# Kernel optimization log

Measured on AMD Instinct MI355X. Metric: run time of the kernel, lower is better.

## Reference

```python
import jax, jax.numpy as jnp
import numpy as np

D_MODEL = 1024
N_HEAD = 16
D_HEAD = D_MODEL // N_HEAD


def setup_inputs() -> dict:
    key = jax.random.key(0)
    k_x, k_wqkv, k_bqkv, k_wp, k_bp = jax.random.split(key, 5)
    B, T = 2, 2048
    bound = 1.0 / np.sqrt(D_MODEL)
    return {
        "x": jax.random.normal(k_x, (B, T, D_MODEL), dtype=jnp.float32),
        "w_qkv": jax.random.uniform(k_wqkv, (D_MODEL, 3 * D_MODEL), jnp.float32, -bound, bound),
        "b_qkv": jax.random.uniform(k_bqkv, (3 * D_MODEL,), jnp.float32, -bound, bound),
        "w_proj": jax.random.uniform(k_wp, (D_MODEL, D_MODEL), jnp.float32, -bound, bound),
        "b_proj": jax.random.uniform(k_bp, (D_MODEL,), jnp.float32, -bound, bound),
    }


def reference(x, w_qkv, b_qkv, w_proj, b_proj):
    B, T, C = x.shape
    qkv = x @ w_qkv + b_qkv                       # [B,T,3C]
    qkv = qkv.reshape(B, T, 3, N_HEAD, D_HEAD)
    qkv = jnp.transpose(qkv, (2, 0, 3, 1, 4))      # [3,B,H,T,dh]
    q, k, v = qkv[0], qkv[1], qkv[2]
    scale = np.sqrt(D_HEAD).astype(np.float32)
    attn = jnp.einsum("bhqd,bhkd->bhqk", q, k) / scale  # [B,H,T,T]
    causal = jnp.tril(jnp.ones((T, T), dtype=bool))
    attn = jnp.where(causal, attn, -jnp.inf)
    attn = jax.nn.softmax(attn, axis=-1)
    out = jnp.einsum("bhqk,bhkd->bhqd", attn, v)   # [B,H,T,dh]
    out = jnp.transpose(out, (0, 2, 1, 3)).reshape(B, T, C)
    return out @ w_proj + b_proj
```

## Files before the change

kernel.cpp:

```cpp
#include <hip/hip_runtime.h>
#include <hip/hip_bf16.h>
#include <math.h>

constexpr int Bb   = 2;
constexpr int T    = 2048;
constexpr int C    = 1024;
constexpr int H    = 16;
constexpr int M    = Bb * T;
constexpr int NQKV = 3 * C;

typedef __attribute__((ext_vector_type(8))) short bf16x8;
typedef __attribute__((ext_vector_type(4))) float f32x4;

__device__ inline short f2bf(float f) {
    __hip_bfloat16 h = __float2bfloat16(f);
    return *reinterpret_cast<short*>(&h);
}

#if __has_builtin(__builtin_amdgcn_exp2f)
#define EXP2(x) __builtin_amdgcn_exp2f(x)
#else
#define EXP2(x) exp2f(x)
#endif

#define GLOBAL_AS __attribute__((address_space(1)))
#define LDS_AS    __attribute__((address_space(3)))

__device__ __forceinline__ void gload_lds16(const short* g, short* s) {
    __builtin_amdgcn_global_load_lds((const GLOBAL_AS void*)g, (LDS_AS void*)s, 16, 0, 0);
}

__global__ __launch_bounds__(256)
void prep_all(const float* __restrict__ x, short* __restrict__ xb,
              const float* __restrict__ w_qkv, short* __restrict__ wqkvt,
              const float* __restrict__ w_proj, short* __restrict__ wprojt)
{
    __shared__ float tile[32][33];
    const int blk = blockIdx.x;
    const int tid = threadIdx.x;

    if (blk < 4096) {
        const int i = blk * 1024 + tid * 4;
        const float4 v = *(const float4*)(x + i);
        short4 s;
        s.x = f2bf(v.x); s.y = f2bf(v.y); s.z = f2bf(v.z); s.w = f2bf(v.w);
        *(short4*)(xb + i) = s;
        return;
    }

    const bool isqkv = (blk < 7168);
    const int bidx = isqkv ? (blk - 4096) : (blk - 7168);
    const int nblk = isqkv ? 96 : 32;
    const int N    = isqkv ? NQKV : C;
    const float* W = isqkv ? w_qkv : w_proj;
    short* Wt      = isqkv ? wqkvt : wprojt;

    const int n0 = (bidx % nblk) * 32, k0 = (bidx / nblk) * 32;
    const int tx = tid & 31, ty = tid >> 5;
#pragma unroll
    for (int i = 0; i < 32; i += 8)
        tile[ty + i][tx] = W[(size_t)(k0 + ty + i) * N + n0 + tx];
    __syncthreads();
#pragma unroll
    for (int i = 0; i < 32; i += 8)
        Wt[(size_t)(n0 + ty + i) * C + k0 + tx] = f2bf(tile[tx][ty + i]);
}

__global__ __launch_bounds__(256)
void gemm_mfma(const short* __restrict__ A, const short* __restrict__ Bt,
               const float* __restrict__ bias, short* __restrict__ outp,
               int Ndim, int Kdim)
{
    __shared__ __align__(16) short As[2 * 128 * 32];
    __shared__ __align__(16) short Bs[2 * 128 * 32];

    const int tid = threadIdx.x;
    const int w   = tid >> 6;
    const int l   = tid & 63;
    const int lk  = l & 15;
    const int lq  = l >> 4;

    const int gx  = gridDim.x;
    const int nwg = gx * gridDim.y;
    const int cpx = nwg >> 3;
    const int bid = blockIdx.y * gx + blockIdx.x;
    const int swz = (bid & 7) * cpx + (bid >> 3);
    const int m0  = (swz / gx) * 128;
    const int n0  = (swz % gx) * 128;

    const int mw  = (w >> 1) * 64, nw = (w & 1) * 64;

    const int srow = w * 16 + (l >> 2);
    const int scol = (l & 3) * 8;

    const short* agp0 = A  + (size_t)(m0 + srow)      * Kdim + scol;
    const short* agp1 = A  + (size_t)(m0 + 64 + srow) * Kdim + scol;
    const short* bgp0 = Bt + (size_t)(n0 + srow)      * Kdim + scol;
    const short* bgp1 = Bt + (size_t)(n0 + 64 + srow) * Kdim + scol;

    short* ad0 = &As[w * 512];
    short* ad1 = &As[2048 + w * 512];
    short* bd0 = &Bs[w * 512];
    short* bd1 = &Bs[2048 + w * 512];

    f32x4 acc[4][4];
#pragma unroll
    for (int i = 0; i < 4; ++i)
#pragma unroll
        for (int j = 0; j < 4; ++j) acc[i][j] = (f32x4){0.f, 0.f, 0.f, 0.f};

    gload_lds16(agp0, ad0);
    gload_lds16(agp1, ad1);
    gload_lds16(bgp0, bd0);
    gload_lds16(bgp1, bd1);
    __syncthreads();

    int cur = 0;
    for (int k0 = 0; k0 < Kdim; k0 += 32) {
        const int coff = cur ? 4096 : 0;

        bf16x8 af[4], bfr[4];
#pragma unroll
        for (int mt = 0; mt < 4; ++mt)
            af[mt] = *(const bf16x8*)&As[coff + (mw + mt * 16 + lk) * 32 + lq * 8];
#pragma unroll
        for (int nt = 0; nt < 4; ++nt)
            bfr[nt] = *(const bf16x8*)&Bs[coff + (nw + nt * 16 + lk) * 32 + lq * 8];

        if (k0 + 32 < Kdim) {
            const int noff = cur ? 0 : 4096;
            gload_lds16(agp0 + k0 + 32, ad0 + noff);
            gload_lds16(agp1 + k0 + 32, ad1 + noff);
            gload_lds16(bgp0 + k0 + 32, bd0 + noff);
            gload_lds16(bgp1 + k0 + 32, bd1 + noff);
        }

#pragma unroll
        for (int mt = 0; mt < 4; ++mt)
#pragma unroll
            for (int nt = 0; nt < 4; ++nt)
                acc[mt][nt] = __builtin_amdgcn_mfma_f32_16x16x32_bf16(bfr[nt], af[mt], acc[mt][nt], 0, 0, 0);

        __syncthreads();
        cur ^= 1;
    }

    float4 bv[4];
#pragma unroll
    for (int nt = 0; nt < 4; ++nt)
        bv[nt] = *(const float4*)(bias + n0 + nw + nt * 16 + lq * 4);
#pragma unroll
    for (int mt = 0; mt < 4; ++mt) {
        short* rowp = outp + (size_t)(m0 + mw + mt * 16 + lk) * Ndim + n0 + nw + lq * 4;
#pragma unroll
        for (int nt = 0; nt < 4; ++nt) {
            short4 pk;
            pk.x = f2bf(acc[mt][nt][0] + bv[nt].x);
            pk.y = f2bf(acc[mt][nt][1] + bv[nt].y);
            pk.z = f2bf(acc[mt][nt][2] + bv[nt].z);
            pk.w = f2bf(acc[mt][nt][3] + bv[nt].w);
            *(short4*)(rowp + nt * 16) = pk;
        }
    }
}

__global__ __launch_bounds__(256)
void gemm_mfma_proj(const short* __restrict__ A, const short* __restrict__ Bt,
                    const float* __restrict__ bias, float* __restrict__ outp,
                    int Ndim, int Kdim)
{
    __shared__ __align__(16) short As[2 * 64 * 32];
    __shared__ __align__(16) short Bs[2 * 128 * 32];

    const int tid = threadIdx.x;
    const int w   = tid >> 6;
    const int l   = tid & 63;
    const int lk  = l & 15;
    const int lq  = l >> 4;

    const int gx  = gridDim.x;
    const int nwg = gx * gridDim.y;
    const int cpx = nwg >> 3;
    const int bid = blockIdx.y * gx + blockIdx.x;
    const int swz = (bid & 7) * cpx + (bid >> 3);
    const int m0  = (swz / gx) * 64;
    const int n0  = (swz % gx) * 128;

    const int mw  = (w & 1) * 32, nw = (w >> 1) * 64;

    const int srow = w * 16 + (l >> 2);
    const int scol = (l & 3) * 8;

    const short* agp  = A  + (size_t)(m0 + srow)      * Kdim + scol;
    const short* bgp0 = Bt + (size_t)(n0 + srow)      * Kdim + scol;
    const short* bgp1 = Bt + (size_t)(n0 + 64 + srow) * Kdim + scol;

    short* ad  = &As[w * 512];
    short* bd0 = &Bs[w * 512];
    short* bd1 = &Bs[2048 + w * 512];

    f32x4 acc[2][4];
#pragma unroll
    for (int i = 0; i < 2; ++i)
#pragma unroll
        for (int j = 0; j < 4; ++j) acc[i][j] = (f32x4){0.f, 0.f, 0.f, 0.f};

    gload_lds16(agp,  ad);
    gload_lds16(bgp0, bd0);
    gload_lds16(bgp1, bd1);
    __syncthreads();

    int cur = 0;
    for (int k0 = 0; k0 < Kdim; k0 += 32) {
        const int coffA = cur ? 2048 : 0;
        const int coffB = cur ? 4096 : 0;

        bf16x8 af[2], bfr[4];
#pragma unroll
        for (int mt = 0; mt < 2; ++mt)
            af[mt] = *(const bf16x8*)&As[coffA + (mw + mt * 16 + lk) * 32 + lq * 8];
#pragma unroll
        for (int nt = 0; nt < 4; ++nt)
            bfr[nt] = *(const bf16x8*)&Bs[coffB + (nw + nt * 16 + lk) * 32 + lq * 8];

        if (k0 + 32 < Kdim) {
            const int noffA = cur ? 0 : 2048;
            const int noffB = cur ? 0 : 4096;
            gload_lds16(agp  + k0 + 32, ad  + noffA);
            gload_lds16(bgp0 + k0 + 32, bd0 + noffB);
            gload_lds16(bgp1 + k0 + 32, bd1 + noffB);
        }

#pragma unroll
        for (int mt = 0; mt < 2; ++mt)
#pragma unroll
            for (int nt = 0; nt < 4; ++nt)
                acc[mt][nt] = __builtin_amdgcn_mfma_f32_16x16x32_bf16(bfr[nt], af[mt], acc[mt][nt], 0, 0, 0);

        __syncthreads();
        cur ^= 1;
    }

    float4 bv[4];
#pragma unroll
    for (int nt = 0; nt < 4; ++nt)
        bv[nt] = *(const float4*)(bias + n0 + nw + nt * 16 + lq * 4);
#pragma unroll
    for (int mt = 0; mt < 2; ++mt) {
        float* rowp = outp + (size_t)(m0 + mw + mt * 16 + lk) * Ndim + n0 + nw + lq * 4;
#pragma unroll
        for (int nt = 0; nt < 4; ++nt) {
            float4 v;
            v.x = acc[mt][nt][0] + bv[nt].x;
            v.y = acc[mt][nt][1] + bv[nt].y;
            v.z = acc[mt][nt][2] + bv[nt].z;
            v.w = acc[mt][nt][3] + bv[nt].w;
            *(float4*)(rowp + nt * 16) = v;
        }
    }
}

constexpr int LDV = 136;
constexpr float SC = 0.18033688f;

__global__ __launch_bounds__(512, 2)
void attn_mfma(const short* __restrict__ qkv, short* __restrict__ att)
{
    __shared__ __align__(16) short Ks[2][128 * 64];
    __shared__ __align__(16) short Vt[2][64 * LDV];

    const int idx = blockIdx.x;
    const int xcd = idx & 7;
    const int r   = idx >> 3;
    const int bh  = xcd * 4 + (r & 3);
    const int s   = r >> 2;
    const int b   = bh >> 4;
    const int h   = bh & 15;

    const int tid = threadIdx.x;
    const int w   = tid >> 6;
    const int l   = tid & 63;
    const int lk  = l & 15;
    const int lq  = l >> 4;

    const short* base = qkv + (size_t)b * T * 3072 + h * 64;

    const int kcolsw = 8 * ((l & 7) ^ (l >> 3));
    const int swz    = lk & 15 & 7;

    const int k2  = tid & 63;
    const int vd0 = (tid >> 6) * 8;
    const int kk   = (2 * k2) & 31;
    const int vcol = ((2 * k2) >> 5) * 32 + ((kk >> 2) & 3) * 8
                   + ((kk >> 4) & 1) * 4 + (kk & 3);

    uint4 va, vb;

    for (int pi = 0; pi < 2; ++pi) {
        const int qt    = pi ? (15 - s) : s;
        const int qbase = qt * 128;
        const int nkt   = qt + 1;

        const int q_abs = qbase + w * 16 + lk;
        const short* qp = base + (size_t)q_abs * 3072 + lq * 8;
        const bf16x8 qf0 = *(const bf16x8*)qp;
        const bf16x8 qf1 = *(const bf16x8*)(qp + 32);

        f32x4 acc_o[4];
#pragma unroll
        for (int dt = 0; dt < 4; ++dt) acc_o[dt] = (f32x4){0.f, 0.f, 0.f, 0.f};
        float m_run = -INFINITY;
        float l_run = 0.f;

        __syncthreads();
#pragma unroll
        for (int rr = 0; rr < 2; ++rr) {
            const int rowbase = rr * 64 + w * 8;
            gload_lds16(base + 1024 + (size_t)(rowbase + (l >> 3)) * 3072 + kcolsw,
                        &Ks[0][rowbase * 64]);
        }
        {
            const short* vp = base + 2048 + (size_t)(2 * k2) * 3072 + vd0;
            va = *(const uint4*)vp;
            vb = *(const uint4*)(vp + 3072);
            const unsigned int Aa[4] = {va.x, va.y, va.z, va.w};
            const unsigned int Bbv[4] = {vb.x, vb.y, vb.z, vb.w};
#pragma unroll
            for (int p = 0; p < 4; ++p) {
                const unsigned int ue = (Aa[p] & 0xffffu) | (Bbv[p] << 16);
                const unsigned int uo = (Aa[p] >> 16) | (Bbv[p] & 0xffff0000u);
                *(unsigned int*)&Vt[0][(vd0 + 2 * p)     * LDV + vcol] = ue;
                *(unsigned int*)&Vt[0][(vd0 + 2 * p + 1) * LDV + vcol] = uo;
            }
        }
        __syncthreads();

#pragma unroll 1
        for (int it = 0; it < nkt; ++it) {
            const int j0  = it * 128;
            const int buf = it & 1;
            const int nb  = buf ^ 1;

            if (it + 1 < nkt) {
                const int j1 = j0 + 128;
#pragma unroll
                for (int rr = 0; rr < 2; ++rr) {
                    const int rowbase = rr * 64 + w * 8;
                    gload_lds16(base + 1024 + (size_t)(j1 + rowbase + (l >> 3)) * 3072 + kcolsw,
                                &Ks[nb][rowbase * 64]);
                }
                const short* vp = base + 2048 + (size_t)(j1 + 2 * k2) * 3072 + vd0;
                va = *(const uint4*)vp;
                vb = *(const uint4*)(vp + 3072);
            }

            f32x4 s4[8];
            __builtin_amdgcn_s_setprio(1);
#pragma unroll
            for (int kt = 0; kt < 8; ++kt) {
                const int row = kt * 16 + lk;
                const bf16x8 kf0 = *(const bf16x8*)&Ks[buf][row * 64 + 8 * (lq ^ swz)];
                const bf16x8 kf1 = *(const bf16x8*)&Ks[buf][row * 64 + 8 * ((lq + 4) ^ swz)];
                f32x4 a = (f32x4){0.f, 0.f, 0.f, 0.f};
                a = __builtin_amdgcn_mfma_f32_16x16x32_bf16(kf0, qf0, a, 0, 0, 0);
                a = __builtin_amdgcn_mfma_f32_16x16x32_bf16(kf1, qf1, a, 0, 0, 0);
                s4[kt] = a;
            }
            __builtin_amdgcn_s_setprio(0);

            if (it == nkt - 1) {
#pragma unroll
                for (int kt = 0; kt < 8; ++kt)
#pragma unroll
                    for (int r2 = 0; r2 < 4; ++r2)
                        if (j0 + kt * 16 + lq * 4 + r2 > q_abs) s4[kt][r2] = -1e30f;
            }

            float tm[8];
#pragma unroll
            for (int kt = 0; kt < 8; ++kt)
                tm[kt] = fmaxf(fmaxf(s4[kt][0], s4[kt][1]), fmaxf(s4[kt][2], s4[kt][3]));
            float mx = fmaxf(fmaxf(fmaxf(tm[0], tm[1]), fmaxf(tm[2], tm[3])),
                             fmaxf(fmaxf(tm[4], tm[5]), fmaxf(tm[6], tm[7])));
            mx = fmaxf(mx, __shfl_xor(mx, 16));
            mx = fmaxf(mx, __shfl_xor(mx, 32));

            const bool grow = __any(mx > m_run);
            float corr = 1.f;
            if (grow) {
                const float mn = fmaxf(m_run, mx);
                corr = EXP2((m_run - mn) * SC);
                m_run = mn;
            }
            const float nmc = -m_run * SC;
#pragma unroll
            for (int kt = 0; kt < 8; ++kt)
#pragma unroll
                for (int r2 = 0; r2 < 4; ++r2)
                    s4[kt][r2] = EXP2(fmaf(s4[kt][r2], SC, nmc));

            float ts[8];
#pragma unroll
            for (int kt = 0; kt < 8; ++kt)
                ts[kt] = (s4[kt][0] + s4[kt][1]) + (s4[kt][2] + s4[kt][3]);
            float ps = ((ts[0] + ts[1]) + (ts[2] + ts[3]))
                     + ((ts[4] + ts[5]) + (ts[6] + ts[7]));
            ps += __shfl_xor(ps, 16);
            ps += __shfl_xor(ps, 32);
            l_run = grow ? (l_run * corr + ps) : (l_run + ps);

            unsigned int d0[8], d1[8];
#pragma unroll
            for (int kt = 0; kt < 8; ++kt) {
                d0[kt] = (unsigned int)(unsigned short)f2bf(s4[kt][0])
                       | ((unsigned int)(unsigned short)f2bf(s4[kt][1]) << 16);
                d1[kt] = (unsigned int)(unsigned short)f2bf(s4[kt][2])
                       | ((unsigned int)(unsigned short)f2bf(s4[kt][3]) << 16);
            }

            if (grow) {
#pragma unroll
                for (int dt = 0; dt < 4; ++dt)
#pragma unroll
                    for (int r2 = 0; r2 < 4; ++r2) acc_o[dt][r2] *= corr;
            }

            __builtin_amdgcn_s_setprio(1);
#pragma unroll
            for (int kc = 0; kc < 4; ++kc) {
                union { unsigned int u[4]; bf16x8 v; } up;
                up.u[0] = d0[kc * 2];
                up.u[1] = d1[kc * 2];
                up.u[2] = d0[kc * 2 + 1];
                up.u[3] = d1[kc * 2 + 1];
                const bf16x8 pf = up.v;
#pragma unroll
                for (int dt = 0; dt < 4; ++dt) {
                    const bf16x8 vf = *(const bf16x8*)&Vt[buf][(dt * 16 + lk) * LDV + kc * 32 + lq * 8];
                    acc_o[dt] = __builtin_amdgcn_mfma_f32_16x16x32_bf16(vf, pf, acc_o[dt], 0, 0, 0);
                }
            }
            __builtin_amdgcn_s_setprio(0);

            if (it + 1 < nkt) {
                const unsigned int Aa[4] = {va.x, va.y, va.z, va.w};
                const unsigned int Bbv[4] = {vb.x, vb.y, vb.z, vb.w};
#pragma unroll
                for (int p = 0; p < 4; ++p) {
                    const unsigned int ue = (Aa[p] & 0xffffu) | (Bbv[p] << 16);
                    const unsigned int uo = (Aa[p] >> 16) | (Bbv[p] & 0xffff0000u);
                    *(unsigned int*)&Vt[nb][(vd0 + 2 * p)     * LDV + vcol] = ue;
                    *(unsigned int*)&Vt[nb][(vd0 + 2 * p + 1) * LDV + vcol] = uo;
                }
            }

            __syncthreads();
        }

        const float inv = 1.f / l_run;
        short* op = att + ((size_t)(b * T + q_abs)) * 1024 + h * 64;
#pragma unroll
        for (int dt = 0; dt < 4; ++dt) {
            short4 pk;
            pk.x = f2bf(acc_o[dt][0] * inv);
            pk.y = f2bf(acc_o[dt][1] * inv);
            pk.z = f2bf(acc_o[dt][2] * inv);
            pk.w = f2bf(acc_o[dt][3] * inv);
            *(short4*)(op + dt * 16 + lq * 4) = pk;
        }
    }
}

extern "C" void kernel_launch(void* const* d_in, const int* in_sizes, int n_in,
                              void* d_out, int out_size, void* d_ws, size_t ws_size,
                              hipStream_t stream)
{
    const float* x      = (const float*)d_in[0];
    const float* w_qkv  = (const float*)d_in[1];
    const float* b_qkv  = (const float*)d_in[2];
    const float* w_proj = (const float*)d_in[3];
    const float* b_proj = (const float*)d_in[4];
    float* out = (float*)d_out;

    short* xb     = (short*)d_ws;
    short* wqkvt  = xb     + (size_t)M * C;
    short* wprojt = wqkvt  + (size_t)NQKV * C;
    short* qkvb   = wprojt + (size_t)C * C;
    short* attb   = qkvb   + (size_t)M * NQKV;

    prep_all<<<8192, 256, 0, stream>>>(x, xb, w_qkv, wqkvt, w_proj, wprojt);
    gemm_mfma<<<dim3(NQKV / 128, M / 128), 256, 0, stream>>>(xb, wqkvt, b_qkv, qkvb, NQKV, C);
    attn_mfma<<<256, 512, 0, stream>>>(qkvb, attb);
    gemm_mfma_proj<<<dim3(C / 128, M / 64), 256, 0, stream>>>(attb, wprojt, b_proj, out, C, C);
}
```

Baseline: 188.0 us.

## Rewrite attention with 32x32x16 MFMA, 4-wave blocks, one q-tile per block

Switches the attention kernel from 16x16x32 to 32x32x16 bf16 MFMA, so each wave owns 32 query rows. Blocks shrink to 256 threads, and the grid doubles to 512 so each block handles one q-tile instead of a balanced pair. The V transpose into LDS now uses an XOR swizzle with no padding, and row reductions need fewer cross-lane shuffles. The goal is to cut LDS traffic and shuffle overhead per FLOP. In exchange, the pairing that balanced causal work within a block is lost and register pressure per wave rises.

```diff
diff --git a/kernel.cpp b/kernel.cpp
--- a/kernel.cpp
+++ b/kernel.cpp
@@ -11,6 +11,7 @@
 
 typedef __attribute__((ext_vector_type(8))) short bf16x8;
 typedef __attribute__((ext_vector_type(4))) float f32x4;
+typedef __attribute__((ext_vector_type(16))) float f32x16;
 
 __device__ inline short f2bf(float f) {
     __hip_bfloat16 h = __float2bfloat16(f);
@@ -260,215 +261,229 @@
     }
 }
 
-constexpr int LDV = 136;
 constexpr float SC = 0.18033688f;
 
-__global__ __launch_bounds__(512, 2)
+__global__ __launch_bounds__(256, 2)
 void attn_mfma(const short* __restrict__ qkv, short* __restrict__ att)
 {
     __shared__ __align__(16) short Ks[2][128 * 64];
-    __shared__ __align__(16) short Vt[2][64 * LDV];
-
-    const int idx = blockIdx.x;
-    const int xcd = idx & 7;
-    const int r   = idx >> 3;
-    const int bh  = xcd * 4 + (r & 3);
-    const int s   = r >> 2;
-    const int b   = bh >> 4;
-    const int h   = bh & 15;
+    __shared__ __align__(16) short Vt[2][64 * 128];
+
+    const int idx  = blockIdx.x;
+    const int half = idx >> 8;
+    const int i    = idx & 255;
+    const int xcd  = i & 7;
+    const int bh   = xcd * 4 + ((i >> 3) & 3);
+    const int s    = i >> 5;
+    const int qt   = half ? (15 - s) : s;
+    const int b    = bh >> 4;
+    const int h    = bh & 15;
+    const int qbase = qt * 128;
+    const int nkt   = qt + 1;
 
     const int tid = threadIdx.x;
     const int w   = tid >> 6;
     const int l   = tid & 63;
-    const int lk  = l & 15;
-    const int lq  = l >> 4;
+    const int c31 = l & 31;
+    const int hi  = l >> 5;
 
     const short* base = qkv + (size_t)b * T * 3072 + h * 64;
 
-    const int kcolsw = 8 * ((l & 7) ^ (l >> 3));
-    const int swz    = lk & 15 & 7;
-
-    const int k2  = tid & 63;
-    const int vd0 = (tid >> 6) * 8;
-    const int kk   = (2 * k2) & 31;
-    const int vcol = ((2 * k2) >> 5) * 32 + ((kk >> 2) & 3) * 8
-                   + ((kk >> 4) & 1) * 4 + (kk & 3);
-
-    uint4 va, vb;
-
-    for (int pi = 0; pi < 2; ++pi) {
-        const int qt    = pi ? (15 - s) : s;
-        const int qbase = qt * 128;
-        const int nkt   = qt + 1;
-
-        const int q_abs = qbase + w * 16 + lk;
-        const short* qp = base + (size_t)q_abs * 3072 + lq * 8;
-        const bf16x8 qf0 = *(const bf16x8*)qp;
-        const bf16x8 qf1 = *(const bf16x8*)(qp + 32);
-
-        f32x4 acc_o[4];
-#pragma unroll
-        for (int dt = 0; dt < 4; ++dt) acc_o[dt] = (f32x4){0.f, 0.f, 0.f, 0.f};
-        float m_run = -INFINITY;
-        float l_run = 0.f;
-
-        __syncthreads();
-#pragma unroll
-        for (int rr = 0; rr < 2; ++rr) {
-            const int rowbase = rr * 64 + w * 8;
-            gload_lds16(base + 1024 + (size_t)(rowbase + (l >> 3)) * 3072 + kcolsw,
-                        &Ks[0][rowbase * 64]);
-        }
-        {
-            const short* vp = base + 2048 + (size_t)(2 * k2) * 3072 + vd0;
-            va = *(const uint4*)vp;
-            vb = *(const uint4*)(vp + 3072);
-            const unsigned int Aa[4] = {va.x, va.y, va.z, va.w};
-            const unsigned int Bbv[4] = {vb.x, vb.y, vb.z, vb.w};
-#pragma unroll
-            for (int p = 0; p < 4; ++p) {
-                const unsigned int ue = (Aa[p] & 0xffffu) | (Bbv[p] << 16);
-                const unsigned int uo = (Aa[p] >> 16) | (Bbv[p] & 0xffff0000u);
-                *(unsigned int*)&Vt[0][(vd0 + 2 * p)     * LDV + vcol] = ue;
-                *(unsigned int*)&Vt[0][(vd0 + 2 * p + 1) * LDV + vcol] = uo;
+    const int q_abs = qbase + w * 32 + c31;
+    const short* qp = base + (size_t)q_abs * 3072 + hi * 8;
+    bf16x8 qf[4];
+#pragma unroll
+    for (int ds = 0; ds < 4; ++ds)
+        qf[ds] = *(const bf16x8*)(qp + ds * 16);
+
+    f32x16 acc_o[2];
+#pragma unroll
+    for (int dt = 0; dt < 2; ++dt)
+#pragma unroll
+        for (int r = 0; r < 16; ++r) acc_o[dt][r] = 0.f;
+    float m_run = -INFINITY;
+    float lacc  = 0.f;
+
+    const int kswz = 8 * ((l & 7) ^ ((l >> 3) & 7));
+
+    const int k0v = 2 * l;
+    const int kk5 = k0v & 31;
+    const int pos = (k0v >> 5) * 32 + ((kk5 >> 4) & 1) * 16 + ((kk5 >> 2) & 1) * 8
+                  + ((kk5 >> 3) & 1) * 4 + (kk5 & 3);
+    const int vg  = pos >> 3;
+    const int vpo = pos & 7;
+    const int seg = w * 16;
+
+    union { uint4 q[2]; unsigned int u[8]; } KA, KB;
+    const int dmask = c31 & 15;
+
+#pragma unroll
+    for (int rr = 0; rr < 4; ++rr) {
+        const int rowbase = rr * 32 + w * 8;
+        gload_lds16(base + 1024 + (size_t)(rowbase + (l >> 3)) * 3072 + kswz,
+                    &Ks[0][rowbase * 64]);
+    }
+    {
+        const short* vp = base + 2048 + (size_t)k0v * 3072 + seg;
+        KA.q[0] = *(const uint4*)vp;
+        KA.q[1] = *(const uint4*)(vp + 8);
+        KB.q[0] = *(const uint4*)(vp + 3072);
+        KB.q[1] = *(const uint4*)(vp + 3080);
+#pragma unroll
+        for (int dd = 0; dd < 16; ++dd) {
+            const unsigned int w0 = KA.u[dd >> 1];
+            const unsigned int w1 = KB.u[dd >> 1];
+            const unsigned int pk = (dd & 1) ? ((w0 >> 16) | (w1 & 0xffff0000u))
+                                             : ((w0 & 0xffffu) | (w1 << 16));
+            *(unsigned int*)&Vt[0][(seg + dd) * 128 + ((vg ^ dd) << 3) + vpo] = pk;
+        }
+    }
+    __syncthreads();
+
+#pragma unroll 1
+    for (int it = 0; it < nkt; ++it) {
+        const int j0  = it * 128;
+        const int buf = it & 1;
+        const int nb  = buf ^ 1;
+
+        if (it + 1 < nkt) {
+            const int j1 = j0 + 128;
+#pragma unroll
+            for (int rr = 0; rr < 4; ++rr) {
+                const int rowbase = rr * 32 + w * 8;
+                gload_lds16(base + 1024 + (size_t)(j1 + rowbase + (l >> 3)) * 3072 + kswz,
+                            &Ks[nb][rowbase * 64]);
             }
-        }
-        __syncthreads();
-
-#pragma unroll 1
-        for (int it = 0; it < nkt; ++it) {
-            const int j0  = it * 128;
-            const int buf = it & 1;
-            const int nb  = buf ^ 1;
-
-            if (it + 1 < nkt) {
-                const int j1 = j0 + 128;
-#pragma unroll
-                for (int rr = 0; rr < 2; ++rr) {
-                    const int rowbase = rr * 64 + w * 8;
-                    gload_lds16(base + 1024 + (size_t)(j1 + rowbase + (l >> 3)) * 3072 + kcolsw,
-                                &Ks[nb][rowbase * 64]);
+            const short* vp = base + 2048 + (size_t)(j1 + k0v) * 3072 + seg;
+            KA.q[0] = *(const uint4*)vp;
+            KA.q[1] = *(const uint4*)(vp + 8);
+            KB.q[0] = *(const uint4*)(vp + 3072);
+            KB.q[1] = *(const uint4*)(vp + 3080);
+        }
+
+        f32x16 s4[4];
+        __builtin_amdgcn_s_setprio(1);
+#pragma unroll
+        for (int kb = 0; kb < 4; ++kb) {
+            const short* krp = &Ks[buf][(kb * 32 + c31) * 64];
+            const int sw = c31 & 7;
+            f32x16 a;
+#pragma unroll
+            for (int r = 0; r < 16; ++r) a[r] = 0.f;
+#pragma unroll
+            for (int ds = 0; ds < 4; ++ds) {
+                const bf16x8 kf = *(const bf16x8*)&krp[((ds * 2 + hi) ^ sw) << 3];
+                a = __builtin_amdgcn_mfma_f32_32x32x16_bf16(kf, qf[ds], a, 0, 0, 0);
+            }
+            s4[kb] = a;
+        }
+        __builtin_amdgcn_s_setprio(0);
+
+        if (it == nkt - 1) {
+#pragma unroll
+            for (int kb = 0; kb < 4; ++kb)
+#pragma unroll
+                for (int r = 0; r < 16; ++r) {
+                    const int key = j0 + kb * 32 + (r & 3) + 8 * (r >> 2) + 4 * hi;
+                    if (key > q_abs) s4[kb][r] = -1e30f;
                 }
-                const short* vp = base + 2048 + (size_t)(j1 + 2 * k2) * 3072 + vd0;
-                va = *(const uint4*)vp;
-                vb = *(const uint4*)(vp + 3072);
-            }
-
-            f32x4 s4[8];
-            __builtin_amdgcn_s_setprio(1);
-#pragma unroll
-            for (int kt = 0; kt < 8; ++kt) {
-                const int row = kt * 16 + lk;
-                const bf16x8 kf0 = *(const bf16x8*)&Ks[buf][row * 64 + 8 * (lq ^ swz)];
-                const bf16x8 kf1 = *(const bf16x8*)&Ks[buf][row * 64 + 8 * ((lq + 4) ^ swz)];
-                f32x4 a = (f32x4){0.f, 0.f, 0.f, 0.f};
-                a = __builtin_amdgcn_mfma_f32_16x16x32_bf16(kf0, qf0, a, 0, 0, 0);
-                a = __builtin_amdgcn_mfma_f32_16x16x32_bf16(kf1, qf1, a, 0, 0, 0);
-                s4[kt] = a;
-            }
-            __builtin_amdgcn_s_setprio(0);
-
-            if (it == nkt - 1) {
-#pragma unroll
-                for (int kt = 0; kt < 8; ++kt)
-#pragma unroll
-                    for (int r2 = 0; r2 < 4; ++r2)
-                        if (j0 + kt * 16 + lq * 4 + r2 > q_abs) s4[kt][r2] = -1e30f;
-            }
-
-            float tm[8];
-#pragma unroll
-            for (int kt = 0; kt < 8; ++kt)
-                tm[kt] = fmaxf(fmaxf(s4[kt][0], s4[kt][1]), fmaxf(s4[kt][2], s4[kt][3]));
-            float mx = fmaxf(fmaxf(fmaxf(tm[0], tm[1]), fmaxf(tm[2], tm[3])),
-                             fmaxf(fmaxf(tm[4], tm[5]), fmaxf(tm[6], tm[7])));
-            mx = fmaxf(mx, __shfl_xor(mx, 16));
-            mx = fmaxf(mx, __shfl_xor(mx, 32));
-
-            const bool grow = __any(mx > m_run);
-            float corr = 1.f;
-            if (grow) {
-                const float mn = fmaxf(m_run, mx);
-                corr = EXP2((m_run - mn) * SC);
-                m_run = mn;
-            }
-            const float nmc = -m_run * SC;
-#pragma unroll
-            for (int kt = 0; kt < 8; ++kt)
-#pragma unroll
-                for (int r2 = 0; r2 < 4; ++r2)
-                    s4[kt][r2] = EXP2(fmaf(s4[kt][r2], SC, nmc));
-
-            float ts[8];
-#pragma unroll
-            for (int kt = 0; kt < 8; ++kt)
-                ts[kt] = (s4[kt][0] + s4[kt][1]) + (s4[kt][2] + s4[kt][3]);
-            float ps = ((ts[0] + ts[1]) + (ts[2] + ts[3]))
-                     + ((ts[4] + ts[5]) + (ts[6] + ts[7]));
-            ps += __shfl_xor(ps, 16);
-            ps += __shfl_xor(ps, 32);
-            l_run = grow ? (l_run * corr + ps) : (l_run + ps);
-
-            unsigned int d0[8], d1[8];
-#pragma unroll
-            for (int kt = 0; kt < 8; ++kt) {
-                d0[kt] = (unsigned int)(unsigned short)f2bf(s4[kt][0])
-                       | ((unsigned int)(unsigned short)f2bf(s4[kt][1]) << 16);
-                d1[kt] = (unsigned int)(unsigned short)f2bf(s4[kt][2])
-                       | ((unsigned int)(unsigned short)f2bf(s4[kt][3]) << 16);
-            }
-
-            if (grow) {
-#pragma unroll
-                for (int dt = 0; dt < 4; ++dt)
-#pragma unroll
-                    for (int r2 = 0; r2 < 4; ++r2) acc_o[dt][r2] *= corr;
-            }
-
-            __builtin_amdgcn_s_setprio(1);
-#pragma unroll
-            for (int kc = 0; kc < 4; ++kc) {
+        }
+
+        float tm[4];
+#pragma unroll
+        for (int kb = 0; kb < 4; ++kb) {
+            float a0 = fmaxf(fmaxf(s4[kb][0], s4[kb][1]), fmaxf(s4[kb][2], s4[kb][3]));
+            float a1 = fmaxf(fmaxf(s4[kb][4], s4[kb][5]), fmaxf(s4[kb][6], s4[kb][7]));
+            float a2 = fmaxf(fmaxf(s4[kb][8], s4[kb][9]), fmaxf(s4[kb][10], s4[kb][11]));
+            float a3 = fmaxf(fmaxf(s4[kb][12], s4[kb][13]), fmaxf(s4[kb][14], s4[kb][15]));
+            tm[kb] = fmaxf(fmaxf(a0, a1), fmaxf(a2, a3));
+        }
+        float mx = fmaxf(fmaxf(tm[0], tm[1]), fmaxf(tm[2], tm[3]));
+        mx = fmaxf(mx, __shfl_xor(mx, 32));
+
+        const bool grow = __any(mx > m_run);
+        float corr = 1.f;
+        if (grow) {
+            const float mn = fmaxf(m_run, mx);
+            corr = EXP2((m_run - mn) * SC);
+            m_run = mn;
+        }
+        const float nmc = -m_run * SC;
+#pragma unroll
+        for (int kb = 0; kb < 4; ++kb)
+#pragma unroll
+            for (int r = 0; r < 16; ++r)
+                s4[kb][r] = EXP2(fmaf(s4[kb][r], SC, nmc));
+
+        float ts[4];
+#pragma unroll
+        for (int kb = 0; kb < 4; ++kb) {
+            float a0 = (s4[kb][0] + s4[kb][1]) + (s4[kb][2] + s4[kb][3]);
+            float a1 = (s4[kb][4] + s4[kb][5]) + (s4[kb][6] + s4[kb][7]);
+            float a2 = (s4[kb][8] + s4[kb][9]) + (s4[kb][10] + s4[kb][11]);
+            float a3 = (s4[kb][12] + s4[kb][13]) + (s4[kb][14] + s4[kb][15]);
+            ts[kb] = (a0 + a1) + (a2 + a3);
+        }
+        const float ps = (ts[0] + ts[1]) + (ts[2] + ts[3]);
+        lacc = grow ? (lacc * corr + ps) : (lacc + ps);
+
+        if (grow) {
+#pragma unroll
+            for (int dt = 0; dt < 2; ++dt)
+#pragma unroll
+                for (int r = 0; r < 16; ++r) acc_o[dt][r] *= corr;
+        }
+
+        __builtin_amdgcn_s_setprio(1);
+#pragma unroll
+        for (int kb = 0; kb < 4; ++kb) {
+#pragma unroll
+            for (int hh = 0; hh < 2; ++hh) {
                 union { unsigned int u[4]; bf16x8 v; } up;
-                up.u[0] = d0[kc * 2];
-                up.u[1] = d1[kc * 2];
-                up.u[2] = d0[kc * 2 + 1];
-                up.u[3] = d1[kc * 2 + 1];
-                const bf16x8 pf = up.v;
-#pragma unroll
-                for (int dt = 0; dt < 4; ++dt) {
-                    const bf16x8 vf = *(const bf16x8*)&Vt[buf][(dt * 16 + lk) * LDV + kc * 32 + lq * 8];
-                    acc_o[dt] = __builtin_amdgcn_mfma_f32_16x16x32_bf16(vf, pf, acc_o[dt], 0, 0, 0);
+#pragma unroll
+                for (int p = 0; p < 4; ++p)
+                    up.u[p] = (unsigned int)(unsigned short)f2bf(s4[kb][hh * 8 + 2 * p])
+                            | ((unsigned int)(unsigned short)f2bf(s4[kb][hh * 8 + 2 * p + 1]) << 16);
+                const int g = kb * 4 + hh * 2 + hi;
+#pragma unroll
+                for (int dt = 0; dt < 2; ++dt) {
+                    const bf16x8 vf = *(const bf16x8*)
+                        &Vt[buf][(dt * 32 + c31) * 128 + ((g ^ dmask) << 3)];
+                    acc_o[dt] = __builtin_amdgcn_mfma_f32_32x32x16_bf16(vf, up.v, acc_o[dt], 0, 0, 0);
                 }
             }
-            __builtin_amdgcn_s_setprio(0);
-
-            if (it + 1 < nkt) {
-                const unsigned int Aa[4] = {va.x, va.y, va.z, va.w};
-                const unsigned int Bbv[4] = {vb.x, vb.y, vb.z, vb.w};
-#pragma unroll
-                for (int p = 0; p < 4; ++p) {
-                    const unsigned int ue = (Aa[p] & 0xffffu) | (Bbv[p] << 16);
-                    const unsigned int uo = (Aa[p] >> 16) | (Bbv[p] & 0xffff0000u);
-                    *(unsigned int*)&Vt[nb][(vd0 + 2 * p)     * LDV + vcol] = ue;
-                    *(unsigned int*)&Vt[nb][(vd0 + 2 * p + 1) * LDV + vcol] = uo;
-                }
+        }
+        __builtin_amdgcn_s_setprio(0);
+
+        if (it + 1 < nkt) {
+#pragma unroll
+            for (int dd = 0; dd < 16; ++dd) {
+                const unsigned int w0 = KA.u[dd >> 1];
+                const unsigned int w1 = KB.u[dd >> 1];
+                const unsigned int pk = (dd & 1) ? ((w0 >> 16) | (w1 & 0xffff0000u))
+                                                 : ((w0 & 0xffffu) | (w1 << 16));
+                *(unsigned int*)&Vt[nb][(seg + dd) * 128 + ((vg ^ dd) << 3) + vpo] = pk;
             }
-
-            __syncthreads();
-        }
-
-        const float inv = 1.f / l_run;
-        short* op = att + ((size_t)(b * T + q_abs)) * 1024 + h * 64;
-#pragma unroll
-        for (int dt = 0; dt < 4; ++dt) {
+        }
+
+        __syncthreads();
+    }
+
+    const float ls  = lacc + __shfl_xor(lacc, 32);
+    const float inv = 1.f / ls;
+    short* op = att + ((size_t)(b * T + q_abs)) * 1024 + h * 64;
+#pragma unroll
+    for (int dt = 0; dt < 2; ++dt)
+#pragma unroll
+        for (int rg = 0; rg < 4; ++rg) {
+            const int d0 = dt * 32 + 8 * rg + 4 * hi;
             short4 pk;
-            pk.x = f2bf(acc_o[dt][0] * inv);
-            pk.y = f2bf(acc_o[dt][1] * inv);
-            pk.z = f2bf(acc_o[dt][2] * inv);
-            pk.w = f2bf(acc_o[dt][3] * inv);
-            *(short4*)(op + dt * 16 + lq * 4) = pk;
-        }
-    }
+            pk.x = f2bf(acc_o[dt][rg * 4 + 0] * inv);
+            pk.y = f2bf(acc_o[dt][rg * 4 + 1] * inv);
+            pk.z = f2bf(acc_o[dt][rg * 4 + 2] * inv);
+            pk.w = f2bf(acc_o[dt][rg * 4 + 3] * inv);
+            *(short4*)(op + d0) = pk;
+        }
 }
 
 extern "C" void kernel_launch(void* const* d_in, const int* in_sizes, int n_in,
@@ -490,6 +505,6 @@
 
     prep_all<<<8192, 256, 0, stream>>>(x, xb, w_qkv, wqkvt, w_proj, wprojt);
     gemm_mfma<<<dim3(NQKV / 128, M / 128), 256, 0, stream>>>(xb, wqkvt, b_qkv, qkvb, NQKV, C);
-    attn_mfma<<<256, 512, 0, stream>>>(qkvb, attb);
+    attn_mfma<<<512, 256, 0, stream>>>(qkvb, attb);
     gemm_mfma_proj<<<dim3(C / 128, M / 64), 256, 0, stream>>>(attb, wprojt, b_proj, out, C, C);
 }
```

Measured after the change: 196.8 us. 1.05x slower.

## Use persistent attention blocks with atomic work queue and smaller 64-row tiles

Applied to the files above, without the earlier changes.

Restructures the attention kernel from a fixed pairing of 128-row query tiles (s and 15-s) across 256 blocks of 512 threads into 768 persistent blocks of 256 threads. Each block processes 64-query, 64-key tiles and pulls further work units from a global atomic counter, ordered longest-first. The counter is zeroed in the prep kernel. The aim is better load balancing of the causal triangle and higher occupancy. The cost is smaller tiles with less reuse per block, more synchronisation per key tile, and the overhead of the atomic.

```diff
diff --git a/kernel.cpp b/kernel.cpp
--- a/kernel.cpp
+++ b/kernel.cpp
@@ -33,11 +33,14 @@
 __global__ __launch_bounds__(256)
 void prep_all(const float* __restrict__ x, short* __restrict__ xb,
               const float* __restrict__ w_qkv, short* __restrict__ wqkvt,
-              const float* __restrict__ w_proj, short* __restrict__ wprojt)
+              const float* __restrict__ w_proj, short* __restrict__ wprojt,
+              int* __restrict__ qcnt)
 {
     __shared__ float tile[32][33];
     const int blk = blockIdx.x;
     const int tid = threadIdx.x;
+
+    if (blk == 0 && tid == 0) *qcnt = 0;
 
     if (blk < 4096) {
         const int i = blk * 1024 + tid * 4;
@@ -260,22 +263,18 @@
     }
 }
 
-constexpr int LDV = 136;
+constexpr int LDV = 104;
 constexpr float SC = 0.18033688f;
-
-__global__ __launch_bounds__(512, 2)
-void attn_mfma(const short* __restrict__ qkv, short* __restrict__ att)
+constexpr int NUNITS = 1024;
+constexpr int NBLK   = 768;
+
+__global__ __launch_bounds__(256, 3)
+void attn_mfma(const short* __restrict__ qkv, short* __restrict__ att,
+               int* __restrict__ qcnt)
 {
-    __shared__ __align__(16) short Ks[2][128 * 64];
+    __shared__ __align__(16) short Ks[2][64 * 64];
     __shared__ __align__(16) short Vt[2][64 * LDV];
-
-    const int idx = blockIdx.x;
-    const int xcd = idx & 7;
-    const int r   = idx >> 3;
-    const int bh  = xcd * 4 + (r & 3);
-    const int s   = r >> 2;
-    const int b   = bh >> 4;
-    const int h   = bh & 15;
+    __shared__ int s_unit;
 
     const int tid = threadIdx.x;
     const int w   = tid >> 6;
@@ -283,23 +282,28 @@
     const int lk  = l & 15;
     const int lq  = l >> 4;
 
-    const short* base = qkv + (size_t)b * T * 3072 + h * 64;
-
-    const int kcolsw = 8 * ((l & 7) ^ (l >> 3));
-    const int swz    = lk & 15 & 7;
-
-    const int k2  = tid & 63;
-    const int vd0 = (tid >> 6) * 8;
-    const int kk   = (2 * k2) & 31;
-    const int vcol = ((2 * k2) >> 5) * 32 + ((kk >> 2) & 3) * 8
-                   + ((kk >> 4) & 1) * 4 + (kk & 3);
+    const int kswz = 8 * ((l & 7) ^ (l >> 3));
+    const int swz  = lk & 7;
+
+    const int k2  = tid & 31;
+    const int vd0 = (tid >> 5) * 8;
+    const int kk  = 2 * k2;
+    const int w5  = kk & 31;
+    const int vcol = (kk >> 5) * 32 + ((w5 >> 2) & 3) * 8
+                   + ((w5 >> 4) & 1) * 4 + (w5 & 3);
 
     uint4 va, vb;
 
-    for (int pi = 0; pi < 2; ++pi) {
-        const int qt    = pi ? (15 - s) : s;
-        const int qbase = qt * 128;
+    int unit = blockIdx.x;
+    while (true) {
+        const int qt = 31 - (unit >> 5);
+        const int bh = unit & 31;
+        const int b  = bh >> 4;
+        const int h  = bh & 15;
+        const int qbase = qt * 64;
         const int nkt   = qt + 1;
+
+        const short* base = qkv + (size_t)b * T * 3072 + h * 64;
 
         const int q_abs = qbase + w * 16 + lk;
         const short* qp = base + (size_t)q_abs * 3072 + lq * 8;
@@ -312,23 +316,22 @@
         float m_run = -INFINITY;
         float l_run = 0.f;
 
-        __syncthreads();
 #pragma unroll
         for (int rr = 0; rr < 2; ++rr) {
-            const int rowbase = rr * 64 + w * 8;
-            gload_lds16(base + 1024 + (size_t)(rowbase + (l >> 3)) * 3072 + kcolsw,
+            const int rowbase = rr * 32 + w * 8;
+            gload_lds16(base + 1024 + (size_t)(rowbase + (l >> 3)) * 3072 + kswz,
                         &Ks[0][rowbase * 64]);
         }
         {
-            const short* vp = base + 2048 + (size_t)(2 * k2) * 3072 + vd0;
+            const short* vp = base + 2048 + (size_t)kk * 3072 + vd0;
             va = *(const uint4*)vp;
             vb = *(const uint4*)(vp + 3072);
             const unsigned int Aa[4] = {va.x, va.y, va.z, va.w};
-            const unsigned int Bbv[4] = {vb.x, vb.y, vb.z, vb.w};
+            const unsigned int Bv[4] = {vb.x, vb.y, vb.z, vb.w};
 #pragma unroll
             for (int p = 0; p < 4; ++p) {
-                const unsigned int ue = (Aa[p] & 0xffffu) | (Bbv[p] << 16);
-                const unsigned int uo = (Aa[p] >> 16) | (Bbv[p] & 0xffff0000u);
+                const unsigned int ue = (Aa[p] & 0xffffu) | (Bv[p] << 16);
+                const unsigned int uo = (Aa[p] >> 16) | (Bv[p] & 0xffff0000u);
                 *(unsigned int*)&Vt[0][(vd0 + 2 * p)     * LDV + vcol] = ue;
                 *(unsigned int*)&Vt[0][(vd0 + 2 * p + 1) * LDV + vcol] = uo;
             }
@@ -337,27 +340,27 @@
 
 #pragma unroll 1
         for (int it = 0; it < nkt; ++it) {
-            const int j0  = it * 128;
+            const int j0  = it * 64;
             const int buf = it & 1;
             const int nb  = buf ^ 1;
 
             if (it + 1 < nkt) {
-                const int j1 = j0 + 128;
+                const int j1 = j0 + 64;
 #pragma unroll
                 for (int rr = 0; rr < 2; ++rr) {
-                    const int rowbase = rr * 64 + w * 8;
-                    gload_lds16(base + 1024 + (size_t)(j1 + rowbase + (l >> 3)) * 3072 + kcolsw,
+                    const int rowbase = rr * 32 + w * 8;
+                    gload_lds16(base + 1024 + (size_t)(j1 + rowbase + (l >> 3)) * 3072 + kswz,
                                 &Ks[nb][rowbase * 64]);
                 }
-                const short* vp = base + 2048 + (size_t)(j1 + 2 * k2) * 3072 + vd0;
+                const short* vp = base + 2048 + (size_t)(j1 + kk) * 3072 + vd0;
                 va = *(const uint4*)vp;
                 vb = *(const uint4*)(vp + 3072);
             }
 
-            f32x4 s4[8];
+            f32x4 s4[4];
             __builtin_amdgcn_s_setprio(1);
 #pragma unroll
-            for (int kt = 0; kt < 8; ++kt) {
+            for (int kt = 0; kt < 4; ++kt) {
                 const int row = kt * 16 + lk;
                 const bf16x8 kf0 = *(const bf16x8*)&Ks[buf][row * 64 + 8 * (lq ^ swz)];
                 const bf16x8 kf1 = *(const bf16x8*)&Ks[buf][row * 64 + 8 * ((lq + 4) ^ swz)];
@@ -370,18 +373,17 @@
 
             if (it == nkt - 1) {
 #pragma unroll
-                for (int kt = 0; kt < 8; ++kt)
+                for (int kt = 0; kt < 4; ++kt)
 #pragma unroll
                     for (int r2 = 0; r2 < 4; ++r2)
                         if (j0 + kt * 16 + lq * 4 + r2 > q_abs) s4[kt][r2] = -1e30f;
             }
 
-            float tm[8];
-#pragma unroll
-            for (int kt = 0; kt < 8; ++kt)
+            float tm[4];
+#pragma unroll
+            for (int kt = 0; kt < 4; ++kt)
                 tm[kt] = fmaxf(fmaxf(s4[kt][0], s4[kt][1]), fmaxf(s4[kt][2], s4[kt][3]));
-            float mx = fmaxf(fmaxf(fmaxf(tm[0], tm[1]), fmaxf(tm[2], tm[3])),
-                             fmaxf(fmaxf(tm[4], tm[5]), fmaxf(tm[6], tm[7])));
+            float mx = fmaxf(fmaxf(tm[0], tm[1]), fmaxf(tm[2], tm[3]));
             mx = fmaxf(mx, __shfl_xor(mx, 16));
             mx = fmaxf(mx, __shfl_xor(mx, 32));
 
@@ -394,24 +396,23 @@
             }
             const float nmc = -m_run * SC;
 #pragma unroll
-            for (int kt = 0; kt < 8; ++kt)
+            for (int kt = 0; kt < 4; ++kt)
 #pragma unroll
                 for (int r2 = 0; r2 < 4; ++r2)
                     s4[kt][r2] = EXP2(fmaf(s4[kt][r2], SC, nmc));
 
-            float ts[8];
-#pragma unroll
-            for (int kt = 0; kt < 8; ++kt)
+            float ts[4];
+#pragma unroll
+            for (int kt = 0; kt < 4; ++kt)
                 ts[kt] = (s4[kt][0] + s4[kt][1]) + (s4[kt][2] + s4[kt][3]);
-            float ps = ((ts[0] + ts[1]) + (ts[2] + ts[3]))
-                     + ((ts[4] + ts[5]) + (ts[6] + ts[7]));
+            float ps = (ts[0] + ts[1]) + (ts[2] + ts[3]);
             ps += __shfl_xor(ps, 16);
             ps += __shfl_xor(ps, 32);
             l_run = grow ? (l_run * corr + ps) : (l_run + ps);
 
-            unsigned int d0[8], d1[8];
-#pragma unroll
-            for (int kt = 0; kt < 8; ++kt) {
+            unsigned int d0[4], d1[4];
+#pragma unroll
+            for (int kt = 0; kt < 4; ++kt) {
                 d0[kt] = (unsigned int)(unsigned short)f2bf(s4[kt][0])
                        | ((unsigned int)(unsigned short)f2bf(s4[kt][1]) << 16);
                 d1[kt] = (unsigned int)(unsigned short)f2bf(s4[kt][2])
@@ -427,7 +428,7 @@
 
             __builtin_amdgcn_s_setprio(1);
 #pragma unroll
-            for (int kc = 0; kc < 4; ++kc) {
+            for (int kc = 0; kc < 2; ++kc) {
                 union { unsigned int u[4]; bf16x8 v; } up;
                 up.u[0] = d0[kc * 2];
                 up.u[1] = d1[kc * 2];
@@ -444,11 +445,11 @@
 
             if (it + 1 < nkt) {
                 const unsigned int Aa[4] = {va.x, va.y, va.z, va.w};
-                const unsigned int Bbv[4] = {vb.x, vb.y, vb.z, vb.w};
+                const unsigned int Bv[4] = {vb.x, vb.y, vb.z, vb.w};
 #pragma unroll
                 for (int p = 0; p < 4; ++p) {
-                    const unsigned int ue = (Aa[p] & 0xffffu) | (Bbv[p] << 16);
-                    const unsigned int uo = (Aa[p] >> 16) | (Bbv[p] & 0xffff0000u);
+                    const unsigned int ue = (Aa[p] & 0xffffu) | (Bv[p] << 16);
+                    const unsigned int uo = (Aa[p] >> 16) | (Bv[p] & 0xffff0000u);
                     *(unsigned int*)&Vt[nb][(vd0 + 2 * p)     * LDV + vcol] = ue;
                     *(unsigned int*)&Vt[nb][(vd0 + 2 * p + 1) * LDV + vcol] = uo;
                 }
@@ -468,6 +469,11 @@
             pk.w = f2bf(acc_o[dt][3] * inv);
             *(short4*)(op + dt * 16 + lq * 4) = pk;
         }
+
+        if (tid == 0) s_unit = NBLK + atomicAdd(qcnt, 1);
+        __syncthreads();
+        unit = s_unit;
+        if (unit >= NUNITS) break;
     }
 }
 
@@ -487,9 +493,10 @@
     short* wprojt = wqkvt  + (size_t)NQKV * C;
     short* qkvb   = wprojt + (size_t)C * C;
     short* attb   = qkvb   + (size_t)M * NQKV;
-
-    prep_all<<<8192, 256, 0, stream>>>(x, xb, w_qkv, wqkvt, w_proj, wprojt);
+    int*   qcnt   = (int*)(attb + (size_t)M * C);
+
+    prep_all<<<8192, 256, 0, stream>>>(x, xb, w_qkv, wqkvt, w_proj, wprojt, qcnt);
     gemm_mfma<<<dim3(NQKV / 128, M / 128), 256, 0, stream>>>(xb, wqkvt, b_qkv, qkvb, NQKV, C);
-    attn_mfma<<<256, 512, 0, stream>>>(qkvb, attb);
+    attn_mfma<<<NBLK, 256, 0, stream>>>(qkvb, attb, qcnt);
     gemm_mfma_proj<<<dim3(C / 128, M / 64), 256, 0, stream>>>(attb, wprojt, b_proj, out, C, C);
 }
```

Result: no change. 186.9 us (-0.6%).
